# Kernel optimization log

Measured on AMD Instinct MI355X. Metric: run time of the kernel, lower is better.

The kernel has to match this reference:

```python
import jax, jax.numpy as jnp
import numpy as np

STATE_DIM = 128
N_RBF = 20
R_CUT = 10.0
N_NODES = 25000
N_EDGES = 250000
N_GRAPHS = 512
N_ATOMS = 100
NUM_ROUNDS = 1


def setup_inputs() -> dict:
    key = jax.random.key(0)
    ks = jax.random.split(key, 20)
    D = STATE_DIM

    def w(k, shape, s=0.05):
        return jax.random.normal(k, shape, jnp.float32) * s

    return {
        "edge_vec": jax.random.normal(ks[0], (N_EDGES, 3), jnp.float32),
        "embedding": w(ks[1], (N_ATOMS, D), 1.0),
        "phi_W1": w(ks[2], (D, D)), "phi_b1": jnp.zeros((D,), jnp.float32),
        "phi_W2": w(ks[3], (D, 3 * D)), "phi_b2": jnp.zeros((3 * D,), jnp.float32),
        "filt_W": w(ks[4], (N_RBF, 3 * D)), "filt_b": jnp.zeros((3 * D,), jnp.float32),
        "upd_W1": w(ks[5], (2 * D, D)), "upd_b1": jnp.zeros((D,), jnp.float32),
        "upd_W2": w(ks[6], (D, 3 * D)), "upd_b2": jnp.zeros((3 * D,), jnp.float32),
        "out_W1": w(ks[7], (D, D)), "out_b1": jnp.zeros((D,), jnp.float32),
        "out_W2": w(ks[8], (D, 1)), "out_b2": jnp.zeros((1,), jnp.float32),
        "U_W": w(ks[9], (D, D)),
        "V_W": w(ks[10], (D, D)),
        "atom_types": jax.random.randint(ks[11], (N_NODES,), 0, N_ATOMS),
        "node_from": jax.random.randint(ks[12], (N_EDGES,), 0, N_NODES),
        "node_to": jax.random.randint(ks[13], (N_EDGES,), 0, N_NODES),
        "node_graph_index": jnp.sort(jax.random.randint(ks[14], (N_NODES,), 0, N_GRAPHS)),
        "num_graphs": N_GRAPHS,
    }


def _painn_forward(edge_vec, embedding, phi_W1, phi_b1, phi_W2, phi_b2,
                   filt_W, filt_b, upd_W1, upd_b1, upd_W2, upd_b2,
                   out_W1, out_b1, out_W2, out_b2, U_W, V_W,
                   atom_types, node_from, node_to, node_graph_index, num_graphs):
    silu = jax.nn.silu
    D = STATE_DIM
    # initial node scalar states from atom-type embedding; vector states zero
    state = embedding[atom_types]                         # [N, D]
    state_vec = jnp.zeros((state.shape[0], 3, D), state.dtype)  # [N, 3, D]

    # edge geometry (constant across rounds)
    d = jnp.linalg.norm(edge_vec, axis=1, keepdims=True)  # [E, 1]
    kfreq = jnp.arange(1, N_RBF + 1, dtype=jnp.float32)   # PaiNN sinc radial basis
    rbf = jnp.sin(kfreq * jnp.pi * d / R_CUT) / d         # [E, n]
    fc = 0.5 * (jnp.cos(jnp.pi * d / R_CUT) + 1.0) * (d < R_CUT)  # cosine cutoff [E,1]
    W_out = (rbf @ filt_W + filt_b) * fc                  # [E, 3D]
    normalized = edge_vec / d                             # [E, 3]

    for _ in range(NUM_ROUNDS):
        # --- message block ---
        inp = state[node_from]                             # gather [E, D]
        phi = silu(inp @ phi_W1 + phi_b1) @ phi_W2 + phi_b2  # [E, 3D]
        pf = phi * W_out                                   # [E, 3D]
        m1, m2, m3 = pf[:, :D], pf[:, D:2 * D], pf[:, 2 * D:]
        msg_vec = (state_vec[node_from] * m1[:, None, :]
                   + normalized[:, :, None] * m3[:, None, :])  # [E, 3, D]
        state = state.at[node_to].add(m2)                  # scatter-add scalars
        state_vec = state_vec.at[node_to].add(msg_vec)     # scatter-add vectors

        # --- update block (torch detaches state_vec here) ---
        sv = jax.lax.stop_gradient(state_vec)
        Up = sv @ U_W                                      # [N, 3, D]
        Vp = sv @ V_W                                      # [N, 3, D]
        UV = jnp.sum(Up * Vp, axis=1)                      # [N, D]
        Vn = jnp.linalg.norm(Vp, axis=1)                   # [N, D]
        h = jnp.concatenate([Vn, state], axis=1)           # [N, 2D]
        a = silu(h @ upd_W1 + upd_b1) @ upd_W2 + upd_b2    # [N, 3D]
        a_vv, a_sv, a_ss = a[:, :D], a[:, D:2 * D], a[:, 2 * D:]
        state = state + a_ss + UV * a_sv
        state_vec = state_vec + Up * a_vv[:, None, :]

    idx = node_graph_index - node_graph_index[0]
    graph_state = jax.ops.segment_sum(state, idx, num_segments=num_graphs)  # [G, D]
    return silu(graph_state @ out_W1 + out_b1) @ out_W2 + out_b2            # [G, 1]


def reference(edge_vec, embedding, phi_W1, phi_b1, phi_W2, phi_b2,
              filt_W, filt_b, upd_W1, upd_b1, upd_W2, upd_b2,
              out_W1, out_b1, out_W2, out_b2, U_W, V_W,
              atom_types, node_from, node_to, node_graph_index, num_graphs):
    return _painn_forward(edge_vec, embedding, phi_W1, phi_b1, phi_W2, phi_b2,
                          filt_W, filt_b, upd_W1, upd_b1, upd_W2, upd_b2,
                          out_W1, out_b1, out_W2, out_b2, U_W, V_W,
                          atom_types, node_from, node_to, node_graph_index, num_graphs)
```

## Files before the change

kernel.cpp:

```cpp
#include <hip/hip_runtime.h>
#include <math.h>

#define D 128
#define NRBF 20
#define NEDGES 250000
#define NNODES 25000
#define NGRAPHS 512
#define NATOMS 100

constexpr float RCUT = 10.0f;
constexpr float PI_F = 3.14159265358979323846f;

__device__ __forceinline__ float silu_f(float x) { return x / (1.0f + __expf(-x)); }

__global__ __launch_bounds__(128) void k_phi_table(
    const float* __restrict__ emb, const float* __restrict__ W1, const float* __restrict__ b1,
    const float* __restrict__ W2, const float* __restrict__ b2, float* __restrict__ phi_tab)
{
    __shared__ float s_in[D];
    __shared__ float s_hid[D];
    const int t = blockIdx.x;
    const int j = threadIdx.x;
    s_in[j] = emb[t * D + j];
    __syncthreads();
    float acc = b1[j];
    for (int c = 0; c < D; ++c) acc = fmaf(s_in[c], W1[c * D + j], acc);
    s_hid[j] = silu_f(acc);
    __syncthreads();
    #pragma unroll
    for (int r = 0; r < 3; ++r) {
        const int col = r * D + j;
        float a2 = b2[col];
        for (int c = 0; c < D; ++c) a2 = fmaf(s_hid[c], W2[c * 384 + col], a2);
        phi_tab[t * 384 + col] = a2;
    }
}

__global__ void k_zero(int* __restrict__ counts, int* __restrict__ glo, int* __restrict__ ghi)
{
    const int i = blockIdx.x * 256 + threadIdx.x;
    if (i < NNODES) counts[i] = 0;
    if (i < NGRAPHS) { glo[i] = 0x7fffffff; ghi[i] = -1; }
}

__global__ void k_hist(const int* __restrict__ node_to, int* __restrict__ counts,
                       const int* __restrict__ ngi, int* __restrict__ glo, int* __restrict__ ghi)
{
    const int e = blockIdx.x * 256 + threadIdx.x;
    if (e < NEDGES) atomicAdd(&counts[node_to[e]], 1);
    if (e < NNODES) {
        const int g = ngi[e] - ngi[0];
        atomicMin(&glo[g], e);
        atomicMax(&ghi[g], e);
    }
}

__global__ __launch_bounds__(1024) void k_scan(int* __restrict__ counts,
                                               int* __restrict__ row_ptr)
{
    __shared__ int s[1024];
    const int t = threadIdx.x;
    const int base = t * 25;
    int sum = 0;
    for (int j = 0; j < 25; ++j) {
        const int idx = base + j;
        if (idx < NNODES) sum += counts[idx];
    }
    s[t] = sum;
    __syncthreads();
    for (int off = 1; off < 1024; off <<= 1) {
        int v = 0;
        if (t >= off) v = s[t - off];
        __syncthreads();
        if (t >= off) s[t] += v;
        __syncthreads();
    }
    int run = (t > 0) ? s[t - 1] : 0;
    for (int j = 0; j < 25; ++j) {
        const int idx = base + j;
        if (idx < NNODES) {
            const int v = counts[idx];
            row_ptr[idx] = run;
            counts[idx] = run;
            run += v;
        }
    }
    if (t == 1023) row_ptr[NNODES] = s[1023];
}

__global__ __launch_bounds__(256) void k_pre(
    const float* __restrict__ edge_vec, const int* __restrict__ node_from,
    const int* __restrict__ node_to, const int* __restrict__ atom_types,
    int* __restrict__ cursor, float* __restrict__ edata, int* __restrict__ ety)
{
    const int e = blockIdx.x * 256 + threadIdx.x;
    if (e >= NEDGES) return;
    const float x = edge_vec[e * 3 + 0];
    const float y = edge_vec[e * 3 + 1];
    const float z = edge_vec[e * 3 + 2];
    const float d = sqrtf(x * x + y * y + z * z);
    const float inv = 1.0f / d;
    const float th = PI_F * d / RCUT;
    const float fc = (d < RCUT) ? 0.5f * (__cosf(th) + 1.0f) : 0.0f;
    const float sc = fc * inv;

    float buf[24];
    #pragma unroll
    for (int k = 0; k < NRBF; ++k) buf[k] = __sinf((float)(k + 1) * th) * sc;
    buf[20] = fc;
    buf[21] = x * inv;
    buf[22] = y * inv;
    buf[23] = z * inv;

    const int slot = atomicAdd(&cursor[node_to[e]], 1);
    float* o = edata + (size_t)slot * 24;
    #pragma unroll
    for (int q = 0; q < 6; ++q) *(float4*)(o + q * 4) = *(float4*)&buf[q * 4];
    ety[slot] = atom_types[node_from[e]];
}

#define GNPB 16
#define CHUNK 64
__global__ __launch_bounds__(128, 4) void k_gather(
    const int* __restrict__ row_ptr, const float* __restrict__ edata,
    const int* __restrict__ ety, const float* __restrict__ phi_tab,
    const float* __restrict__ filt_W, const float* __restrict__ filt_b,
    const float* __restrict__ emb, const int* __restrict__ atom_types,
    float* __restrict__ state, float* __restrict__ sv)
{
    __shared__ __align__(16) float s_ed[CHUNK * 24];
    __shared__ int s_ep[CHUNK];
    __shared__ int s_rp[GNPB + 1];

    const int t = threadIdx.x;
    const int c1 = 128 + t;
    const int c2 = 256 + t;

    const int n0 = blockIdx.x * GNPB;
    const int nEnd = min(n0 + GNPB, NNODES);
    if (t <= GNPB) s_rp[t] = row_ptr[min(n0 + t, NNODES)];

    float fw1[NRBF], fw2[NRBF];
    #pragma unroll
    for (int k = 0; k < NRBF; ++k) {
        fw1[k] = filt_W[k * 384 + c1];
        fw2[k] = filt_W[k * 384 + c2];
    }
    const float fb1 = filt_b[c1];
    const float fb2 = filt_b[c2];

    __syncthreads();
    const int e0 = s_rp[0];
    const int e1 = s_rp[nEnd - n0];

    int cur = n0;
    int nb = s_rp[1];
    float s0 = 0.f, v0 = 0.f, v1 = 0.f, v2 = 0.f;

    auto flush = [&]() {
        state[cur * D + t] = emb[atom_types[cur] * D + t] + s0;
        float* b = sv + (size_t)cur * 3 * D + t;
        b[0] = v0; b[128] = v1; b[256] = v2;
        s0 = v0 = v1 = v2 = 0.f;
        ++cur;
        nb = s_rp[cur - n0 + 1];
    };

    for (int base = e0; base < e1; base += CHUNK) {
        const int cnt = min(CHUNK, e1 - base);
        __syncthreads();
        for (int i = t; i < cnt * 6; i += 128)
            ((float4*)s_ed)[i] = ((const float4*)edata)[(size_t)base * 6 + i];
        for (int i = t; i < cnt; i += 128) s_ep[i] = ety[base + i];
        __syncthreads();

        int j = 0;
        while (j < cnt) {
            while (base + j >= nb) flush();
            const int lim = min(nb - base, cnt);
            int ty = s_ep[j];
            float p1 = phi_tab[ty * 384 + c1];
            float p2 = phi_tab[ty * 384 + c2];
            #pragma unroll 2
            for (; j < lim; ++j) {
                const float cp1 = p1, cp2 = p2;
                if (j + 1 < cnt) {
                    const int tyn = s_ep[j + 1];
                    p1 = phi_tab[tyn * 384 + c1];
                    p2 = phi_tab[tyn * 384 + c2];
                }
                const float4* p = (const float4*)(s_ed + j * 24);
                const float4 q0 = p[0], q1 = p[1], q2 = p[2], q3 = p[3], q4 = p[4], q5 = p[5];
                float wa1 = fb1 * q5.x,      wb1 = q2.z * fw1[10];
                float wa2 = fb2 * q5.x,      wb2 = q2.z * fw2[10];
                wa1 = fmaf(q0.x, fw1[0], wa1);  wb1 = fmaf(q2.w, fw1[11], wb1);
                wa2 = fmaf(q0.x, fw2[0], wa2);  wb2 = fmaf(q2.w, fw2[11], wb2);
                wa1 = fmaf(q0.y, fw1[1], wa1);  wb1 = fmaf(q3.x, fw1[12], wb1);
                wa2 = fmaf(q0.y, fw2[1], wa2);  wb2 = fmaf(q3.x, fw2[12], wb2);
                wa1 = fmaf(q0.z, fw1[2], wa1);  wb1 = fmaf(q3.y, fw1[13], wb1);
                wa2 = fmaf(q0.z, fw2[2], wa2);  wb2 = fmaf(q3.y, fw2[13], wb2);
                wa1 = fmaf(q0.w, fw1[3], wa1);  wb1 = fmaf(q3.z, fw1[14], wb1);
                wa2 = fmaf(q0.w, fw2[3], wa2);  wb2 = fmaf(q3.z, fw2[14], wb2);
                wa1 = fmaf(q1.x, fw1[4], wa1);  wb1 = fmaf(q3.w, fw1[15], wb1);
                wa2 = fmaf(q1.x, fw2[4], wa2);  wb2 = fmaf(q3.w, fw2[15], wb2);
                wa1 = fmaf(q1.y, fw1[5], wa1);  wb1 = fmaf(q4.x, fw1[16], wb1);
                wa2 = fmaf(q1.y, fw2[5], wa2);  wb2 = fmaf(q4.x, fw2[16], wb2);
                wa1 = fmaf(q1.z, fw1[6], wa1);  wb1 = fmaf(q4.y, fw1[17], wb1);
                wa2 = fmaf(q1.z, fw2[6], wa2);  wb2 = fmaf(q4.y, fw2[17], wb2);
                wa1 = fmaf(q1.w, fw1[7], wa1);  wb1 = fmaf(q4.z, fw1[18], wb1);
                wa2 = fmaf(q1.w, fw2[7], wa2);  wb2 = fmaf(q4.z, fw2[18], wb2);
                wa1 = fmaf(q2.x, fw1[8], wa1);  wb1 = fmaf(q4.w, fw1[19], wb1);
                wa2 = fmaf(q2.x, fw2[8], wa2);  wb2 = fmaf(q4.w, fw2[19], wb2);
                wa1 = fmaf(q2.y, fw1[9], wa1);
                wa2 = fmaf(q2.y, fw2[9], wa2);
                const float pf1 = cp1 * (wa1 + wb1);
                const float pf2 = cp2 * (wa2 + wb2);
                s0 += pf1;
                v0 = fmaf(q5.y, pf2, v0);
                v1 = fmaf(q5.z, pf2, v1);
                v2 = fmaf(q5.w, pf2, v2);
            }
        }
    }
    while (cur < nEnd) flush();
}

#define UVBN 64
__global__ __launch_bounds__(256) void k_uv(
    const float* __restrict__ sv, const float* __restrict__ U_W, const float* __restrict__ V_W,
    float* __restrict__ UVb, float* __restrict__ Vnb)
{
    __shared__ float s_x[UVBN][33];
    __shared__ __align__(16) float s_u[32][128];
    __shared__ __align__(16) float s_v[32][128];
    const int t = threadIdx.x;
    const int cg = t & 15;
    const int rg = t >> 4;
    const int n0 = blockIdx.x * UVBN;

    float uvacc[4][8], vnacc[4][8];
    #pragma unroll
    for (int r = 0; r < 4; ++r)
        #pragma unroll
        for (int h = 0; h < 8; ++h) { uvacc[r][h] = 0.f; vnacc[r][h] = 0.f; }

    for (int a = 0; a < 3; ++a) {
        float up[4][8], vp[4][8];
        #pragma unroll
        for (int r = 0; r < 4; ++r)
            #pragma unroll
            for (int h = 0; h < 8; ++h) { up[r][h] = 0.f; vp[r][h] = 0.f; }

        for (int kt = 0; kt < 4; ++kt) {
            __syncthreads();
            for (int i = t; i < UVBN * 32; i += 256) {
                const int row = i >> 5, col = i & 31;
                float xv = 0.f;
                if (n0 + row < NNODES)
                    xv = sv[(size_t)(n0 + row) * 384 + a * 128 + kt * 32 + col];
                s_x[row][col] = xv;
            }
            #pragma unroll
            for (int q = 0; q < 4; ++q) {
                const int i = t + q * 256;
                const int row = i >> 5, col = (i & 31) * 4;
                *(float4*)&s_u[row][col] = *(const float4*)(U_W + (kt * 32 + row) * 128 + col);
                *(float4*)&s_v[row][col] = *(const float4*)(V_W + (kt * 32 + row) * 128 + col);
            }
            __syncthreads();
            #pragma unroll 4
            for (int k = 0; k < 32; ++k) {
                const float4 ua = *(const float4*)&s_u[k][cg * 4];
                const float4 ub = *(const float4*)&s_u[k][64 + cg * 4];
                const float4 va = *(const float4*)&s_v[k][cg * 4];
                const float4 vb = *(const float4*)&s_v[k][64 + cg * 4];
                #pragma unroll
                for (int r = 0; r < 4; ++r) {
                    const float x = s_x[rg * 4 + r][k];
                    up[r][0] = fmaf(x, ua.x, up[r][0]); up[r][1] = fmaf(x, ua.y, up[r][1]);
                    up[r][2] = fmaf(x, ua.z, up[r][2]); up[r][3] = fmaf(x, ua.w, up[r][3]);
                    up[r][4] = fmaf(x, ub.x, up[r][4]); up[r][5] = fmaf(x, ub.y, up[r][5]);
                    up[r][6] = fmaf(x, ub.z, up[r][6]); up[r][7] = fmaf(x, ub.w, up[r][7]);
                    vp[r][0] = fmaf(x, va.x, vp[r][0]); vp[r][1] = fmaf(x, va.y, vp[r][1]);
                    vp[r][2] = fmaf(x, va.z, vp[r][2]); vp[r][3] = fmaf(x, va.w, vp[r][3]);
                    vp[r][4] = fmaf(x, vb.x, vp[r][4]); vp[r][5] = fmaf(x, vb.y, vp[r][5]);
                    vp[r][6] = fmaf(x, vb.z, vp[r][6]); vp[r][7] = fmaf(x, vb.w, vp[r][7]);
                }
            }
        }
        #pragma unroll
        for (int r = 0; r < 4; ++r)
            #pragma unroll
            for (int h = 0; h < 8; ++h) {
                uvacc[r][h] = fmaf(up[r][h], vp[r][h], uvacc[r][h]);
                vnacc[r][h] = fmaf(vp[r][h], vp[r][h], vnacc[r][h]);
            }
    }

    #pragma unroll
    for (int r = 0; r < 4; ++r) {
        const int n = n0 + rg * 4 + r;
        if (n < NNODES) {
            float vn[8];
            #pragma unroll
            for (int h = 0; h < 8; ++h) vn[h] = sqrtf(vnacc[r][h]);
            *(float4*)(UVb + (size_t)n * D + cg * 4)      = *(float4*)&uvacc[r][0];
            *(float4*)(UVb + (size_t)n * D + 64 + cg * 4) = *(float4*)&uvacc[r][4];
            *(float4*)(Vnb + (size_t)n * D + cg * 4)      = *(float4*)&vn[0];
            *(float4*)(Vnb + (size_t)n * D + 64 + cg * 4) = *(float4*)&vn[4];
        }
    }
}

#define BN1 64
__global__ __launch_bounds__(256) void k_mlp1(
    const float* __restrict__ Vnb, const float* __restrict__ state,
    const float* __restrict__ W1, const float* __restrict__ b1,
    float* __restrict__ hid)
{
    __shared__ float s_h[BN1][33];
    __shared__ __align__(16) float s_w[32][128];
    const int t = threadIdx.x;
    const int cg = t & 15;
    const int rg = t >> 4;
    const int n0 = blockIdx.x * BN1;

    float acc[4][8];
    #pragma unroll
    for (int r = 0; r < 4; ++r)
        #pragma unroll
        for (int h = 0; h < 8; ++h)
            acc[r][h] = (h < 4) ? b1[cg * 4 + h] : b1[64 + cg * 4 + (h - 4)];

    for (int kt = 0; kt < 8; ++kt) {
        const float* src = (kt < 4) ? (Vnb + kt * 32) : (state + (kt - 4) * 32);
        __syncthreads();
        for (int i = t; i < BN1 * 32; i += 256) {
            const int row = i >> 5, col = i & 31;
            float v = 0.f;
            if (n0 + row < NNODES) v = src[(size_t)(n0 + row) * D + col];
            s_h[row][col] = v;
        }
        #pragma unroll
        for (int q = 0; q < 4; ++q) {
            const int i = t + q * 256;
            const int row = i >> 5, col = (i & 31) * 4;
            *(float4*)&s_w[row][col] = *(const float4*)(W1 + (kt * 32 + row) * 128 + col);
        }
        __syncthreads();
        #pragma unroll 8
        for (int k = 0; k < 32; ++k) {
            const float4 wa = *(const float4*)&s_w[k][cg * 4];
            const float4 wb = *(const float4*)&s_w[k][64 + cg * 4];
            #pragma unroll
            for (int r = 0; r < 4; ++r) {
                const float x = s_h[rg * 4 + r][k];
                acc[r][0] = fmaf(x, wa.x, acc[r][0]); acc[r][1] = fmaf(x, wa.y, acc[r][1]);
                acc[r][2] = fmaf(x, wa.z, acc[r][2]); acc[r][3] = fmaf(x, wa.w, acc[r][3]);
                acc[r][4] = fmaf(x, wb.x, acc[r][4]); acc[r][5] = fmaf(x, wb.y, acc[r][5]);
                acc[r][6] = fmaf(x, wb.z, acc[r][6]); acc[r][7] = fmaf(x, wb.w, acc[r][7]);
            }
        }
    }

    #pragma unroll
    for (int r = 0; r < 4; ++r) {
        const int n = n0 + rg * 4 + r;
        if (n < NNODES) {
            float lo[4], hi[4];
            #pragma unroll
            for (int h = 0; h < 4; ++h) { lo[h] = silu_f(acc[r][h]); hi[h] = silu_f(acc[r][h + 4]); }
            *(float4*)(hid + (size_t)n * D + cg * 4)      = *(float4*)lo;
            *(float4*)(hid + (size_t)n * D + 64 + cg * 4) = *(float4*)hi;
        }
    }
}

#define BN2 64
__global__ __launch_bounds__(256) void k_mlp2(
    const float* __restrict__ hid, const float* __restrict__ state,
    const float* __restrict__ UVb,
    const float* __restrict__ W2, const float* __restrict__ b2,
    float* __restrict__ nodeval)
{
    __shared__ float s_h[BN2][33];
    __shared__ __align__(16) float s_w2[32][256];
    const int t = threadIdx.x;
    const int cg = t & 15;
    const int rg = t >> 4;
    const int n0 = blockIdx.x * BN2;

    float acc[4][16];
    #pragma unroll
    for (int r = 0; r < 4; ++r)
        #pragma unroll
        for (int g = 0; g < 4; ++g)
            #pragma unroll
            for (int h = 0; h < 4; ++h)
                acc[r][g * 4 + h] = b2[128 + g * 64 + cg * 4 + h];

    for (int kt = 0; kt < 4; ++kt) {
        __syncthreads();
        for (int i = t; i < BN2 * 32; i += 256) {
            const int row = i >> 5, col = i & 31;
            float v = 0.f;
            if (n0 + row < NNODES) v = hid[(size_t)(n0 + row) * D + kt * 32 + col];
            s_h[row][col] = v;
        }
        #pragma unroll
        for (int q = 0; q < 8; ++q) {
            const int i = t + q * 256;
            const int row = i >> 6, col = (i & 63) * 4;
            *(float4*)&s_w2[row][col] = *(const float4*)(W2 + (kt * 32 + row) * 384 + 128 + col);
        }
        __syncthreads();
        #pragma unroll 4
        for (int k = 0; k < 32; ++k) {
            const float4 w0 = *(const float4*)&s_w2[k][cg * 4];
            const float4 w1 = *(const float4*)&s_w2[k][64 + cg * 4];
            const float4 w2v = *(const float4*)&s_w2[k][128 + cg * 4];
            const float4 w3 = *(const float4*)&s_w2[k][192 + cg * 4];
            #pragma unroll
            for (int r = 0; r < 4; ++r) {
                const float x = s_h[rg * 4 + r][k];
                acc[r][0]  = fmaf(x, w0.x, acc[r][0]);  acc[r][1]  = fmaf(x, w0.y, acc[r][1]);
                acc[r][2]  = fmaf(x, w0.z, acc[r][2]);  acc[r][3]  = fmaf(x, w0.w, acc[r][3]);
                acc[r][4]  = fmaf(x, w1.x, acc[r][4]);  acc[r][5]  = fmaf(x, w1.y, acc[r][5]);
                acc[r][6]  = fmaf(x, w1.z, acc[r][6]);  acc[r][7]  = fmaf(x, w1.w, acc[r][7]);
                acc[r][8]  = fmaf(x, w2v.x, acc[r][8]); acc[r][9]  = fmaf(x, w2v.y, acc[r][9]);
                acc[r][10] = fmaf(x, w2v.z, acc[r][10]);acc[r][11] = fmaf(x, w2v.w, acc[r][11]);
                acc[r][12] = fmaf(x, w3.x, acc[r][12]); acc[r][13] = fmaf(x, w3.y, acc[r][13]);
                acc[r][14] = fmaf(x, w3.z, acc[r][14]); acc[r][15] = fmaf(x, w3.w, acc[r][15]);
            }
        }
    }

    #pragma unroll
    for (int r = 0; r < 4; ++r) {
        const int n = n0 + rg * 4 + r;
        if (n >= NNODES) break;
        const float4 stA = *(const float4*)(state + (size_t)n * D + cg * 4);
        const float4 stB = *(const float4*)(state + (size_t)n * D + 64 + cg * 4);
        const float4 uvA = *(const float4*)(UVb + (size_t)n * D + cg * 4);
        const float4 uvB = *(const float4*)(UVb + (size_t)n * D + 64 + cg * 4);
        float va[4], vb[4];
        va[0] = stA.x + acc[r][8]  + uvA.x * acc[r][0];
        va[1] = stA.y + acc[r][9]  + uvA.y * acc[r][1];
        va[2] = stA.z + acc[r][10] + uvA.z * acc[r][2];
        va[3] = stA.w + acc[r][11] + uvA.w * acc[r][3];
        vb[0] = stB.x + acc[r][12] + uvB.x * acc[r][4];
        vb[1] = stB.y + acc[r][13] + uvB.y * acc[r][5];
        vb[2] = stB.z + acc[r][14] + uvB.z * acc[r][6];
        vb[3] = stB.w + acc[r][15] + uvB.w * acc[r][7];
        *(float4*)(nodeval + (size_t)n * D + cg * 4)      = *(float4*)va;
        *(float4*)(nodeval + (size_t)n * D + 64 + cg * 4) = *(float4*)vb;
    }
}

__global__ __launch_bounds__(128) void k_seg_out(
    const float* __restrict__ nodeval, const int* __restrict__ glo, const int* __restrict__ ghi,
    const float* __restrict__ W1, const float* __restrict__ b1,
    const float* __restrict__ W2, const float* __restrict__ b2, float* __restrict__ out)
{
    __shared__ float s_g[D];
    __shared__ float s_part[2];
    const int g = blockIdx.x;
    const int j = threadIdx.x;
    const int lo = glo[g];
    const int hi = ghi[g];
    float s = 0.f;
    #pragma unroll 4
    for (int n = lo; n <= hi; ++n) s += nodeval[(size_t)n * D + j];
    s_g[j] = s;
    __syncthreads();
    float acc = b1[j];
    for (int c = 0; c < D; ++c) acc = fmaf(s_g[c], W1[c * D + j], acc);
    float m = silu_f(acc) * W2[j];
    #pragma unroll
    for (int off = 32; off > 0; off >>= 1) m += __shfl_down(m, off);
    if ((j & 63) == 0) s_part[j >> 6] = m;
    __syncthreads();
    if (j == 0) out[g] = s_part[0] + s_part[1] + b2[0];
}

extern "C" void kernel_launch(void* const* d_in, const int* in_sizes, int n_in,
                              void* d_out, int out_size, void* d_ws, size_t ws_size,
                              hipStream_t stream) {
    const float* edge_vec  = (const float*)d_in[0];
    const float* embedding = (const float*)d_in[1];
    const float* phi_W1    = (const float*)d_in[2];
    const float* phi_b1    = (const float*)d_in[3];
    const float* phi_W2    = (const float*)d_in[4];
    const float* phi_b2    = (const float*)d_in[5];
    const float* filt_W    = (const float*)d_in[6];
    const float* filt_b    = (const float*)d_in[7];
    const float* upd_W1    = (const float*)d_in[8];
    const float* upd_b1    = (const float*)d_in[9];
    const float* upd_W2    = (const float*)d_in[10];
    const float* upd_b2    = (const float*)d_in[11];
    const float* out_W1    = (const float*)d_in[12];
    const float* out_b1    = (const float*)d_in[13];
    const float* out_W2    = (const float*)d_in[14];
    const float* out_b2    = (const float*)d_in[15];
    const float* U_W       = (const float*)d_in[16];
    const float* V_W       = (const float*)d_in[17];
    const int* atom_types  = (const int*)d_in[18];
    const int* node_from   = (const int*)d_in[19];
    const int* node_to     = (const int*)d_in[20];
    const int* ngi         = (const int*)d_in[21];
    float* out = (float*)d_out;

    float* ws = (float*)d_ws;
    float* phi_tab = ws;
    float* state   = phi_tab + NATOMS * 384;
    float* sv      = state + NNODES * D;
    float* meta    = sv + (size_t)NNODES * 3 * D;
    float* scratch = meta + NGRAPHS * D;
    int*   glo     = (int*)meta;
    int*   ghi     = glo + NGRAPHS;
    int*   row_ptr = (int*)scratch;
    int*   counts  = row_ptr + NNODES + 1;
    int*   ety     = counts + NNODES;
    float* edata   = scratch + 300004;
    float* UVb     = scratch;
    float* Vnb     = scratch + NNODES * D;
    float* hid     = sv;
    float* nodeval = sv + NNODES * D;

    k_phi_table<<<NATOMS, 128, 0, stream>>>(embedding, phi_W1, phi_b1, phi_W2, phi_b2, phi_tab);
    k_zero<<<(NNODES + 255) / 256, 256, 0, stream>>>(counts, glo, ghi);
    k_hist<<<(NEDGES + 255) / 256, 256, 0, stream>>>(node_to, counts, ngi, glo, ghi);
    k_scan<<<1, 1024, 0, stream>>>(counts, row_ptr);
    k_pre<<<(NEDGES + 255) / 256, 256, 0, stream>>>(
        edge_vec, node_from, node_to, atom_types, counts, edata, ety);
    k_gather<<<(NNODES + GNPB - 1) / GNPB, 128, 0, stream>>>(
        row_ptr, edata, ety, phi_tab, filt_W, filt_b, embedding, atom_types, state, sv);
    k_uv<<<(NNODES + UVBN - 1) / UVBN, 256, 0, stream>>>(sv, U_W, V_W, UVb, Vnb);
    k_mlp1<<<(NNODES + BN1 - 1) / BN1, 256, 0, stream>>>(Vnb, state, upd_W1, upd_b1, hid);
    k_mlp2<<<(NNODES + BN2 - 1) / BN2, 256, 0, stream>>>(hid, state, UVb, upd_W2, upd_b2, nodeval);
    k_seg_out<<<NGRAPHS, 128, 0, stream>>>(nodeval, glo, ghi, out_W1, out_b1, out_W2, out_b2, out);
}
```

Measured before the change: 488.6 us.

## Restructure U/V projection kernel to process all three vector components per node

Reorganizes k_uv so each thread owns one node and keeps accumulators for all three spatial components, instead of four nodes looped over components one at a time. Each U/V weight tile is now loaded once per k-step and reused for the three components, rather than reloaded per component. The node tile per block drops from 64 to 16, which launches about four times as many blocks to fill the GPU better. In exchange, each block amortizes weight loads over fewer nodes, so total weight traffic from L2 rises.

Measured after the change: 455.1 us. -6.9%, faster.

```diff
diff --git a/kernel.cpp b/kernel.cpp
--- a/kernel.cpp
+++ b/kernel.cpp
@@ -225,90 +225,79 @@
     while (cur < nEnd) flush();
 }
 
-#define UVBN 64
+#define BNUV 16
 __global__ __launch_bounds__(256) void k_uv(
     const float* __restrict__ sv, const float* __restrict__ U_W, const float* __restrict__ V_W,
     float* __restrict__ UVb, float* __restrict__ Vnb)
 {
-    __shared__ float s_x[UVBN][33];
+    __shared__ __align__(16) float s_sv[BNUV][3][36];
     __shared__ __align__(16) float s_u[32][128];
     __shared__ __align__(16) float s_v[32][128];
     const int t = threadIdx.x;
     const int cg = t & 15;
-    const int rg = t >> 4;
-    const int n0 = blockIdx.x * UVBN;
-
-    float uvacc[4][8], vnacc[4][8];
-    #pragma unroll
-    for (int r = 0; r < 4; ++r)
+    const int ni = t >> 4;
+    const int node0 = blockIdx.x * BNUV;
+
+    float up[3][8], vp[3][8];
+    #pragma unroll
+    for (int a = 0; a < 3; ++a)
         #pragma unroll
-        for (int h = 0; h < 8; ++h) { uvacc[r][h] = 0.f; vnacc[r][h] = 0.f; }
-
-    for (int a = 0; a < 3; ++a) {
-        float up[4][8], vp[4][8];
+        for (int h = 0; h < 8; ++h) { up[a][h] = 0.f; vp[a][h] = 0.f; }
+
+    for (int kt = 0; kt < 4; ++kt) {
+        __syncthreads();
+        for (int i = t; i < 1024; i += 256) {
+            const int row = i >> 5, col = (i & 31) * 4;
+            *(float4*)&s_u[row][col] = *(const float4*)(U_W + (kt * 32 + row) * 128 + col);
+            *(float4*)&s_v[row][col] = *(const float4*)(V_W + (kt * 32 + row) * 128 + col);
+        }
+        for (int i = t; i < 384; i += 256) {
+            const int nd = i / 24;
+            const int rem = i - nd * 24;
+            const int a = rem >> 3, c4 = (rem & 7) * 4;
+            float4 v = make_float4(0.f, 0.f, 0.f, 0.f);
+            if (node0 + nd < NNODES)
+                v = *(const float4*)(sv + (size_t)(node0 + nd) * 384 + a * 128 + kt * 32 + c4);
+            *(float4*)&s_sv[nd][a][c4] = v;
+        }
+        __syncthreads();
+        #pragma unroll 8
+        for (int k = 0; k < 32; ++k) {
+            const float xs0 = s_sv[ni][0][k];
+            const float xs1 = s_sv[ni][1][k];
+            const float xs2 = s_sv[ni][2][k];
+            const float4 ua = *(const float4*)&s_u[k][cg * 4];
+            const float4 ub = *(const float4*)&s_u[k][64 + cg * 4];
+            const float4 va = *(const float4*)&s_v[k][cg * 4];
+            const float4 vb = *(const float4*)&s_v[k][64 + cg * 4];
+            #define UVSTEP(a, XV) \
+                up[a][0] = fmaf(XV, ua.x, up[a][0]); up[a][1] = fmaf(XV, ua.y, up[a][1]); \
+                up[a][2] = fmaf(XV, ua.z, up[a][2]); up[a][3] = fmaf(XV, ua.w, up[a][3]); \
+                up[a][4] = fmaf(XV, ub.x, up[a][4]); up[a][5] = fmaf(XV, ub.y, up[a][5]); \
+                up[a][6] = fmaf(XV, ub.z, up[a][6]); up[a][7] = fmaf(XV, ub.w, up[a][7]); \
+                vp[a][0] = fmaf(XV, va.x, vp[a][0]); vp[a][1] = fmaf(XV, va.y, vp[a][1]); \
+                vp[a][2] = fmaf(XV, va.z, vp[a][2]); vp[a][3] = fmaf(XV, va.w, vp[a][3]); \
+                vp[a][4] = fmaf(XV, vb.x, vp[a][4]); vp[a][5] = fmaf(XV, vb.y, vp[a][5]); \
+                vp[a][6] = fmaf(XV, vb.z, vp[a][6]); vp[a][7] = fmaf(XV, vb.w, vp[a][7]);
+            UVSTEP(0, xs0) UVSTEP(1, xs1) UVSTEP(2, xs2)
+            #undef UVSTEP
+        }
+    }
+
+    const int n = node0 + ni;
+    if (n < NNODES) {
+        float uvr[8], vnr[8];
         #pragma unroll
-        for (int r = 0; r < 4; ++r)
-            #pragma unroll
-            for (int h = 0; h < 8; ++h) { up[r][h] = 0.f; vp[r][h] = 0.f; }
-
-        for (int kt = 0; kt < 4; ++kt) {
-            __syncthreads();
-            for (int i = t; i < UVBN * 32; i += 256) {
-                const int row = i >> 5, col = i & 31;
-                float xv = 0.f;
-                if (n0 + row < NNODES)
-                    xv = sv[(size_t)(n0 + row) * 384 + a * 128 + kt * 32 + col];
-                s_x[row][col] = xv;
-            }
-            #pragma unroll
-            for (int q = 0; q < 4; ++q) {
-                const int i = t + q * 256;
-                const int row = i >> 5, col = (i & 31) * 4;
-                *(float4*)&s_u[row][col] = *(const float4*)(U_W + (kt * 32 + row) * 128 + col);
-                *(float4*)&s_v[row][col] = *(const float4*)(V_W + (kt * 32 + row) * 128 + col);
-            }
-            __syncthreads();
-            #pragma unroll 4
-            for (int k = 0; k < 32; ++k) {
-                const float4 ua = *(const float4*)&s_u[k][cg * 4];
-                const float4 ub = *(const float4*)&s_u[k][64 + cg * 4];
-                const float4 va = *(const float4*)&s_v[k][cg * 4];
-                const float4 vb = *(const float4*)&s_v[k][64 + cg * 4];
-                #pragma unroll
-                for (int r = 0; r < 4; ++r) {
-                    const float x = s_x[rg * 4 + r][k];
-                    up[r][0] = fmaf(x, ua.x, up[r][0]); up[r][1] = fmaf(x, ua.y, up[r][1]);
-                    up[r][2] = fmaf(x, ua.z, up[r][2]); up[r][3] = fmaf(x, ua.w, up[r][3]);
-                    up[r][4] = fmaf(x, ub.x, up[r][4]); up[r][5] = fmaf(x, ub.y, up[r][5]);
-                    up[r][6] = fmaf(x, ub.z, up[r][6]); up[r][7] = fmaf(x, ub.w, up[r][7]);
-                    vp[r][0] = fmaf(x, va.x, vp[r][0]); vp[r][1] = fmaf(x, va.y, vp[r][1]);
-                    vp[r][2] = fmaf(x, va.z, vp[r][2]); vp[r][3] = fmaf(x, va.w, vp[r][3]);
-                    vp[r][4] = fmaf(x, vb.x, vp[r][4]); vp[r][5] = fmaf(x, vb.y, vp[r][5]);
-                    vp[r][6] = fmaf(x, vb.z, vp[r][6]); vp[r][7] = fmaf(x, vb.w, vp[r][7]);
-                }
-            }
-        }
-        #pragma unroll
-        for (int r = 0; r < 4; ++r)
-            #pragma unroll
-            for (int h = 0; h < 8; ++h) {
-                uvacc[r][h] = fmaf(up[r][h], vp[r][h], uvacc[r][h]);
-                vnacc[r][h] = fmaf(vp[r][h], vp[r][h], vnacc[r][h]);
-            }
-    }
-
-    #pragma unroll
-    for (int r = 0; r < 4; ++r) {
-        const int n = n0 + rg * 4 + r;
-        if (n < NNODES) {
-            float vn[8];
-            #pragma unroll
-            for (int h = 0; h < 8; ++h) vn[h] = sqrtf(vnacc[r][h]);
-            *(float4*)(UVb + (size_t)n * D + cg * 4)      = *(float4*)&uvacc[r][0];
-            *(float4*)(UVb + (size_t)n * D + 64 + cg * 4) = *(float4*)&uvacc[r][4];
-            *(float4*)(Vnb + (size_t)n * D + cg * 4)      = *(float4*)&vn[0];
-            *(float4*)(Vnb + (size_t)n * D + 64 + cg * 4) = *(float4*)&vn[4];
-        }
+        for (int h = 0; h < 8; ++h) {
+            uvr[h] = up[0][h] * vp[0][h] + up[1][h] * vp[1][h] + up[2][h] * vp[2][h];
+            vnr[h] = sqrtf(vp[0][h] * vp[0][h] + vp[1][h] * vp[1][h] + vp[2][h] * vp[2][h]);
+        }
+        float* uo = UVb + n * D;
+        float* vo = Vnb + n * D;
+        *(float4*)(uo + cg * 4)      = *(float4*)&uvr[0];
+        *(float4*)(uo + 64 + cg * 4) = *(float4*)&uvr[4];
+        *(float4*)(vo + cg * 4)      = *(float4*)&vnr[0];
+        *(float4*)(vo + 64 + cg * 4) = *(float4*)&vnr[4];
     }
 }
 
@@ -535,7 +524,7 @@
         edge_vec, node_from, node_to, atom_types, counts, edata, ety);
     k_gather<<<(NNODES + GNPB - 1) / GNPB, 128, 0, stream>>>(
         row_ptr, edata, ety, phi_tab, filt_W, filt_b, embedding, atom_types, state, sv);
-    k_uv<<<(NNODES + UVBN - 1) / UVBN, 256, 0, stream>>>(sv, U_W, V_W, UVb, Vnb);
+    k_uv<<<(NNODES + BNUV - 1) / BNUV, 256, 0, stream>>>(sv, U_W, V_W, UVb, Vnb);
     k_mlp1<<<(NNODES + BN1 - 1) / BN1, 256, 0, stream>>>(Vnb, state, upd_W1, upd_b1, hid);
     k_mlp2<<<(NNODES + BN2 - 1) / BN2, 256, 0, stream>>>(hid, state, UVb, upd_W2, upd_b2, nodeval);
     k_seg_out<<<NGRAPHS, 128, 0, stream>>>(nodeval, glo, ghi, out_W1, out_b1, out_W2, out_b2, out);
```
